# Optimization experiments

Measured on AMD Instinct MI355X. Metric: run time of the kernel, lower is better.

The kernel has to match this reference:

```python
import jax, jax.numpy as jnp
import numpy as np

OUT_H, OUT_W = 7, 7
SPATIAL_SCALE = 0.25
SAMPLING_RATIO = 2


def setup_inputs() -> dict:
    key = jax.random.key(0)
    k1, k2, k3 = jax.random.split(key, 3)
    x = jax.random.normal(k1, (4, 256, 200, 200), dtype=jnp.float32)
    bidx = jax.random.randint(k2, (1024,), 0, 4).astype(jnp.float32)
    pts = jax.random.uniform(k3, (1024, 4), jnp.float32, 0.0, 800.0)
    x1 = jnp.minimum(pts[:, 0], pts[:, 2])
    x2 = jnp.maximum(pts[:, 0], pts[:, 2])
    y1 = jnp.minimum(pts[:, 1], pts[:, 3])
    y2 = jnp.maximum(pts[:, 1], pts[:, 3])
    rois = jnp.stack([bidx, x1, y1, x2, y2], axis=1)  # [B,5]
    return {"input": x, "rois": rois}


def reference(input, rois):
    feat = input                                  # [N,C,H,W]
    N, C, H, W = feat.shape
    B = rois.shape[0]
    S = SAMPLING_RATIO
    bi = rois[:, 0].astype(jnp.int32)             # [B] batch index (constant)
    boxes = rois[:, 1:] * SPATIAL_SCALE           # xyxy in feature coords
    rx1, ry1, rx2, ry2 = boxes[:, 0], boxes[:, 1], boxes[:, 2], boxes[:, 3]
    roi_w = jnp.maximum(rx2 - rx1, 1.0)
    roi_h = jnp.maximum(ry2 - ry1, 1.0)
    bin_h = roi_h / OUT_H                         # [B]
    bin_w = roi_w / OUT_W

    # per-ROI continuous sample coordinates: [B, OUT_H*S] and [B, OUT_W*S]
    off_h = (jnp.arange(OUT_H, dtype=jnp.float32)[:, None]
             + (jnp.arange(S, dtype=jnp.float32)[None, :] + 0.5) / S).reshape(-1)
    off_w = (jnp.arange(OUT_W, dtype=jnp.float32)[:, None]
             + (jnp.arange(S, dtype=jnp.float32)[None, :] + 0.5) / S).reshape(-1)
    ys = ry1[:, None] + off_h[None, :] * bin_h[:, None]   # [B, Hs]
    xs = rx1[:, None] + off_w[None, :] * bin_w[:, None]   # [B, Ws]

    # bilinear sampling; pixel i's value sits at continuous coordinate i+0.5
    # (this is the "alignment" handled inside point_interpolate)
    py = jnp.clip(ys - 0.5, 0.0, float(H - 1))
    px = jnp.clip(xs - 0.5, 0.0, float(W - 1))
    y0 = jnp.floor(py).astype(jnp.int32)
    x0 = jnp.floor(px).astype(jnp.int32)
    y1i = jnp.minimum(y0 + 1, H - 1)
    x1i = jnp.minimum(x0 + 1, W - 1)
    wy = (py - y0.astype(py.dtype))[:, :, None, None]     # [B,Hs,1,1]
    wx = (px - x0.astype(px.dtype))[:, None, :, None]     # [B,1,Ws,1]

    b = bi[:, None, None]

    def gather(yy, xx):
        # advanced indexing -> [B, Hs, Ws, C]
        return feat[b, :, yy[:, :, None], xx[:, None, :]]

    v = (gather(y0, x0) * (1.0 - wy) * (1.0 - wx)
         + gather(y0, x1i) * (1.0 - wy) * wx
         + gather(y1i, x0) * wy * (1.0 - wx)
         + gather(y1i, x1i) * wy * wx)                    # [B,Hs,Ws,C]

    # average pool the S x S samples within each output bin
    out = v.reshape(B, OUT_H, S, OUT_W, S, C).mean(axis=(2, 4))  # [B,OH,OW,C]
    return out.transpose(0, 3, 1, 2)                             # [B,C,OH,OW]
```

## Files before the change

kernel.cpp:

```cpp
#include <hip/hip_runtime.h>
#include <hip/hip_bf16.h>

#define CC 256
#define HH 200
#define WW 200
#define PLANE (HH * WW)
#define OUT_H 7
#define OUT_W 7
#define NSP   (OUT_H * OUT_W)

__global__ __launch_bounds__(256) void nchw2nhwc_bf16(const float* __restrict__ in,
                                                      __hip_bfloat16* __restrict__ out)
{
    __shared__ float tile[64][65];
    int n  = blockIdx.z;
    int c0 = blockIdx.y * 64;
    int p0 = blockIdx.x * 64;
    int tx = threadIdx.x & 63;
    int ty = threadIdx.x >> 6;

    const float* src = in + ((size_t)n * CC + c0) * PLANE + p0;
    #pragma unroll
    for (int i = 0; i < 16; ++i) {
        int c = i * 4 + ty;
        tile[c][tx] = src[(size_t)c * PLANE + tx];
    }
    __syncthreads();
    __hip_bfloat16* dst = out + ((size_t)n * PLANE + p0) * CC + c0;
    #pragma unroll
    for (int i = 0; i < 16; ++i) {
        int p = i * 4 + ty;
        dst[(size_t)p * CC + tx] = __float2bfloat16(tile[tx][p]);
    }
}

__global__ __launch_bounds__(256) void roialign_nhwc4_bf16(
    const __hip_bfloat16* __restrict__ nhwc,
    const float* __restrict__ rois,
    float* __restrict__ out)
{
    __shared__ float obuf[64 * NSP];
    int blk = blockIdx.x;
    int b   = blk >> 2;
    int cg  = blk & 3;
    int t   = threadIdx.x;
    int q   = t & 63;
    int wv  = t >> 6;

    const float* r = rois + b * 5;
    int   bi  = (int)r[0];
    float rx1 = r[1] * 0.25f, ry1 = r[2] * 0.25f;
    float rx2 = r[3] * 0.25f, ry2 = r[4] * 0.25f;
    float bin_w = fmaxf(rx2 - rx1, 1.0f) * (1.0f / OUT_W);
    float bin_h = fmaxf(ry2 - ry1, 1.0f) * (1.0f / OUT_H);

    const __hip_bfloat16* base = nhwc + (size_t)bi * PLANE * CC + cg * 64 + q;

    for (int s = wv; s < NSP; s += 4) {
        int pw = s % OUT_W, ph = s / OUT_W;
        float acc = 0.0f;
        #pragma unroll
        for (int iy = 0; iy < 2; ++iy) {
            float yy = ry1 + ((float)ph + ((float)iy + 0.5f) * 0.5f) * bin_h;
            float py = fminf(fmaxf(yy - 0.5f, 0.0f), (float)(HH - 1));
            int   y0 = min((int)py, HH - 2);
            float fy = py - (float)y0;
            #pragma unroll
            for (int ix = 0; ix < 2; ++ix) {
                float xx = rx1 + ((float)pw + ((float)ix + 0.5f) * 0.5f) * bin_w;
                float px = fminf(fmaxf(xx - 0.5f, 0.0f), (float)(WW - 1));
                int   x0 = min((int)px, WW - 2);
                float fx = px - (float)x0;

                const __hip_bfloat16* p00 = base + (size_t)(y0 * WW + x0) * CC;
                float v00 = __bfloat162float(p00[0]);
                float v01 = __bfloat162float(p00[CC]);
                float v10 = __bfloat162float(p00[WW * CC]);
                float v11 = __bfloat162float(p00[WW * CC + CC]);

                acc += v00 * (1.f - fy) * (1.f - fx)
                     + v01 * (1.f - fy) * fx
                     + v10 * fy * (1.f - fx)
                     + v11 * fy * fx;
            }
        }
        obuf[q * NSP + s] = acc * 0.25f;
    }
    __syncthreads();

    float* ob = out + (size_t)b * (CC * NSP) + (size_t)cg * (64 * NSP);
    for (int k = t; k < 64 * NSP; k += 256)
        ob[k] = obuf[k];
}

__global__ __launch_bounds__(256) void roialign_fallback(
    const float* __restrict__ feat, const float* __restrict__ rois,
    float* __restrict__ out, int total)
{
    int idx = blockIdx.x * blockDim.x + threadIdx.x;
    if (idx >= total) return;
    int pw = idx % OUT_W;
    int ph = (idx / OUT_W) % OUT_H;
    int c  = (idx / NSP) % CC;
    int b  = idx / (NSP * CC);

    const float* r = rois + b * 5;
    int   bi  = (int)r[0];
    float rx1 = r[1] * 0.25f, ry1 = r[2] * 0.25f;
    float rx2 = r[3] * 0.25f, ry2 = r[4] * 0.25f;
    float bin_w = fmaxf(rx2 - rx1, 1.0f) * (1.0f / OUT_W);
    float bin_h = fmaxf(ry2 - ry1, 1.0f) * (1.0f / OUT_H);

    const float* fptr = feat + ((size_t)bi * CC + c) * PLANE;
    float acc = 0.0f;
    #pragma unroll
    for (int iy = 0; iy < 2; ++iy) {
        float yy = ry1 + ((float)ph + ((float)iy + 0.5f) * 0.5f) * bin_h;
        float py = fminf(fmaxf(yy - 0.5f, 0.0f), (float)(HH - 1));
        int   y0 = min((int)py, HH - 2);
        float fy = py - (float)y0;
        #pragma unroll
        for (int ix = 0; ix < 2; ++ix) {
            float xx = rx1 + ((float)pw + ((float)ix + 0.5f) * 0.5f) * bin_w;
            float px = fminf(fmaxf(xx - 0.5f, 0.0f), (float)(WW - 1));
            int   x0 = min((int)px, WW - 2);
            float fx = px - (float)x0;
            const float* p = fptr + y0 * WW + x0;
            acc += p[0]      * (1.f - fy) * (1.f - fx)
                 + p[1]      * (1.f - fy) * fx
                 + p[WW]     * fy * (1.f - fx)
                 + p[WW + 1] * fy * fx;
        }
    }
    out[idx] = acc * 0.25f;
}

extern "C" void kernel_launch(void* const* d_in, const int* in_sizes, int n_in,
                              void* d_out, int out_size, void* d_ws, size_t ws_size,
                              hipStream_t stream) {
    const float* feat = (const float*)d_in[0];
    const float* rois = (const float*)d_in[1];
    float* out = (float*)d_out;

    int N = in_sizes[0] / (CC * PLANE);
    int B = in_sizes[1] / 5;

    size_t need = (size_t)N * PLANE * CC * sizeof(__hip_bfloat16);
    if (ws_size >= need) {
        nchw2nhwc_bf16<<<dim3(PLANE / 64, CC / 64, N), 256, 0, stream>>>(
            feat, (__hip_bfloat16*)d_ws);
        roialign_nhwc4_bf16<<<dim3(B * 4), 256, 0, stream>>>(
            (const __hip_bfloat16*)d_ws, rois, out);
    } else {
        int total = out_size;
        roialign_fallback<<<(total + 255) / 256, 256, 0, stream>>>(feat, rois, out, total);
    }
}
```

Baseline: 90.90 us.

## Sort ROIs by batch and Morton order, remap blocks across XCDs for locality

```diff
diff --git a/kernel.cpp b/kernel.cpp
--- a/kernel.cpp
+++ b/kernel.cpp
@@ -8,11 +8,15 @@
 #define OUT_H 7
 #define OUT_W 7
 #define NSP   (OUT_H * OUT_W)
-
-__global__ __launch_bounds__(256) void nchw2nhwc_bf16(const float* __restrict__ in,
-                                                      __hip_bfloat16* __restrict__ out)
+#define BMAX  1024
+
+__global__ __launch_bounds__(256) void nchw2nhwc_bf16_sort(
+    const float* __restrict__ in, __hip_bfloat16* __restrict__ out,
+    const float* __restrict__ rois, int B, unsigned short* __restrict__ perm)
 {
     __shared__ float tile[64][65];
+    __shared__ unsigned skey[BMAX];
+
     int n  = blockIdx.z;
     int c0 = blockIdx.y * 64;
     int p0 = blockIdx.x * 64;
@@ -32,20 +36,65 @@
         int p = i * 4 + ty;
         dst[(size_t)p * CC + tx] = __float2bfloat16(tile[tx][p]);
     }
-}
-
-__global__ __launch_bounds__(256) void roialign_nhwc4_bf16(
+
+    if (blockIdx.x == 0 && blockIdx.y == 0 && blockIdx.z == 0) {
+        int t = threadIdx.x;
+        for (int i = t; i < BMAX; i += 256) {
+            unsigned k = 0xFFFFFFFFu;
+            if (i < B) {
+                const float* r = rois + i * 5;
+                unsigned bi = (unsigned)(int)r[0];
+                float cx = (r[1] + r[3]) * 0.125f;
+                float cy = (r[2] + r[4]) * 0.125f;
+                unsigned ix = (unsigned)fminf(fmaxf(cx, 0.f), 255.f);
+                unsigned iy = (unsigned)fminf(fmaxf(cy, 0.f), 255.f);
+                unsigned m = 0;
+                #pragma unroll
+                for (int bp = 0; bp < 8; ++bp) {
+                    m |= ((ix >> bp) & 1u) << (2 * bp);
+                    m |= ((iy >> bp) & 1u) << (2 * bp + 1);
+                }
+                k = (bi << 26) | (m << 10) | (unsigned)i;
+            }
+            skey[i] = k;
+        }
+        __syncthreads();
+        for (int size = 2; size <= BMAX; size <<= 1) {
+            for (int stride = size >> 1; stride > 0; stride >>= 1) {
+                for (int i = t; i < BMAX; i += 256) {
+                    int p = i ^ stride;
+                    if (p > i) {
+                        bool up = ((i & size) == 0);
+                        unsigned a = skey[i], b2 = skey[p];
+                        if ((a > b2) == up) { skey[i] = b2; skey[p] = a; }
+                    }
+                }
+                __syncthreads();
+            }
+        }
+        for (int i = t; i < BMAX; i += 256) perm[i] = (unsigned short)(skey[i] & 1023u);
+    }
+}
+
+__global__ __launch_bounds__(256) void roialign_nhwc4_bf16s(
     const __hip_bfloat16* __restrict__ nhwc,
     const float* __restrict__ rois,
+    const unsigned short* __restrict__ perm,
     float* __restrict__ out)
 {
     __shared__ float obuf[64 * NSP];
-    int blk = blockIdx.x;
-    int b   = blk >> 2;
-    int cg  = blk & 3;
-    int t   = threadIdx.x;
-    int q   = t & 63;
-    int wv  = t >> 6;
+    int nblk = gridDim.x;
+    int bid  = blockIdx.x;
+    int pos;
+    if ((nblk & 7) == 0) { int cpx = nblk >> 3; pos = (bid & 7) * cpx + (bid >> 3); }
+    else                 { pos = bid; }
+    int slot = pos >> 2;
+    int cg   = pos & 3;
+    int b    = (int)perm[slot];
+
+    int t  = threadIdx.x;
+    int q  = t & 63;
+    int wv = t >> 6;
 
     const float* r = rois + b * 5;
     int   bi  = (int)r[0];
@@ -145,12 +194,15 @@
     int N = in_sizes[0] / (CC * PLANE);
     int B = in_sizes[1] / 5;
 
-    size_t need = (size_t)N * PLANE * CC * sizeof(__hip_bfloat16);
-    if (ws_size >= need) {
-        nchw2nhwc_bf16<<<dim3(PLANE / 64, CC / 64, N), 256, 0, stream>>>(
-            feat, (__hip_bfloat16*)d_ws);
-        roialign_nhwc4_bf16<<<dim3(B * 4), 256, 0, stream>>>(
-            (const __hip_bfloat16*)d_ws, rois, out);
+    size_t nhwc_bytes = (size_t)N * PLANE * CC * sizeof(__hip_bfloat16);
+    size_t need = nhwc_bytes + BMAX * sizeof(unsigned short);
+
+    if (ws_size >= need && B <= BMAX) {
+        __hip_bfloat16* nhwc = (__hip_bfloat16*)d_ws;
+        unsigned short* perm = (unsigned short*)((char*)d_ws + nhwc_bytes);
+        nchw2nhwc_bf16_sort<<<dim3(PLANE / 64, CC / 64, N), 256, 0, stream>>>(
+            feat, nhwc, rois, B, perm);
+        roialign_nhwc4_bf16s<<<dim3(B * 4), 256, 0, stream>>>(nhwc, rois, perm, out);
     } else {
         int total = out_size;
         roialign_fallback<<<(total + 255) / 256, 256, 0, stream>>>(feat, rois, out, total);
```

Result: faster. 84.50 us (-7.0%).
